# Optimization experiments

Hardware: AMD Instinct MI355X
Metric: run time of the kernel (lower is better)

Reference implementation:

```python
import jax, jax.numpy as jnp
import numpy as np

N_NODES = 50000
N_EDGES = 800000
HEADS = 2
HID = 64
NEG_SLOPE = 0.2


def setup_inputs() -> dict:
    key = jax.random.key(0)
    ks = jax.random.split(key, 8)
    x = jax.random.normal(ks[0], (N_NODES, 128), dtype=jnp.float32)
    W_src = jax.random.normal(ks[1], (128, HEADS * HID), dtype=jnp.float32) * (1.0 / np.sqrt(128))
    W_dst = jax.random.normal(ks[2], (128, HEADS * HID), dtype=jnp.float32) * (1.0 / np.sqrt(128))
    att_src = jax.random.normal(ks[3], (HEADS, HID), dtype=jnp.float32) * 0.1
    att_dst = jax.random.normal(ks[4], (HEADS, HID), dtype=jnp.float32) * 0.1
    bias = jax.random.normal(ks[5], (HEADS * HID,), dtype=jnp.float32) * 0.01
    prelu_w = jnp.full((HEADS * HID,), 0.25, dtype=jnp.float32)
    edge_index = jax.random.randint(ks[6], (2, N_EDGES), 0, N_NODES, dtype=jnp.int64)
    return {"x": x, "W_src": W_src, "W_dst": W_dst, "att_src": att_src,
            "att_dst": att_dst, "bias": bias, "prelu_w": prelu_w,
            "edge_index": edge_index}


def gat_prelu(x, W_src, W_dst, att_src, att_dst, bias, prelu_w, edge_index):
    N = x.shape[0]
    src, dst = edge_index[0], edge_index[1]
    xs = (x @ W_src).reshape(N, HEADS, HID)   # [N,H,C]
    xd = (x @ W_dst).reshape(N, HEADS, HID)
    a_src = jnp.einsum('nhc,hc->nh', xs, att_src)  # [N,H]
    a_dst = jnp.einsum('nhc,hc->nh', xd, att_dst)
    e = jax.nn.leaky_relu(a_src[src] + a_dst[dst], NEG_SLOPE)  # [E,H]
    # segment softmax over incoming edges of each dst node
    m = jax.ops.segment_max(e, dst, num_segments=N)            # [N,H]
    ee = jnp.exp(e - m[dst])
    denom = jax.ops.segment_sum(ee, dst, num_segments=N)
    alpha = ee / (denom[dst] + 1e-16)                          # [E,H]
    msg = xs[src] * alpha[:, :, None]                          # [E,H,C]
    out = jax.ops.segment_sum(msg, dst, num_segments=N)        # [N,H,C]
    out = out.reshape(N, HEADS * HID) + bias
    return jnp.where(out >= 0, out, prelu_w * out)


def reference(x, W_src, W_dst, att_src, att_dst, bias, prelu_w, edge_index):
    return gat_prelu(x, W_src, W_dst, att_src, att_dst, bias, prelu_w, edge_index)
```

## Files before the change

### kernel.cpp

```cpp
#include <hip/hip_runtime.h>
#include <hip/hip_fp16.h>


#define N_NODES 50000
#define N_EDGES 800000
#define CAP     56
#define BSH     8
#define NB      196
#define CHUNK   4096
#define NBLK    196
#define CCAP    64

#define OFF_A      0
#define OFF_CNT    800000
#define OFF_XS     1000256
#define OFF_BKT0   13800256
#define OFF_BKT1   25000256
#define OFF_SWZ    36200256
#define DOUT_COARSE 0
#define DOUT_CELL   19668992

typedef _Float16 f16x8 __attribute__((ext_vector_type(8)));
typedef _Float16 f16x4 __attribute__((ext_vector_type(4)));
typedef float    f32x4 __attribute__((ext_vector_type(4)));
typedef int      i32x4 __attribute__((ext_vector_type(4)));
typedef unsigned long long u64;

__global__ __launch_bounds__(256) void k0_prep(
    const float* __restrict__ Wsrc, const float* __restrict__ Wdst,
    const float* __restrict__ att_s, const float* __restrict__ att_d,
    __half* __restrict__ swz)
{
    __shared__ float vS[128 * 4];
    const int nt = blockIdx.x;
    const int t = threadIdx.x;
    if (nt == 8) {
        if (t < 128) {
            const float* wsp = Wsrc + t * 128;
            const float* wdp = Wdst + t * 128;
            float a0 = 0.f, a1 = 0.f, a2 = 0.f, a3 = 0.f;
#pragma unroll 8
            for (int c = 0; c < 64; ++c) {
                a0 += wsp[c]      * att_s[c];
                a1 += wsp[64 + c] * att_s[64 + c];
                a2 += wdp[c]      * att_d[c];
                a3 += wdp[64 + c] * att_d[64 + c];
            }
            *(float4*)(vS + t * 4) = make_float4(a0, a1, a2, a3);
        }
        __syncthreads();
    }
    const int kb = t >> 6, L = t & 63;
    const int col = L & 15;
    const int krow = kb * 32 + ((L >> 4) & 3) * 8;
    f16x8 v;
    if (nt < 8) {
#pragma unroll
        for (int j = 0; j < 8; ++j)
            v[j] = (_Float16)Wsrc[(size_t)(krow + j) * 128 + nt * 16 + col];
    } else {
#pragma unroll
        for (int j = 0; j < 8; ++j)
            v[j] = (col < 4) ? (_Float16)vS[(krow + j) * 4 + col] : (_Float16)0.f;
    }
    *(f16x8*)(swz + ((size_t)(kb * 9 + nt) * 64 + L) * 8) = v;
}

__global__ __launch_bounds__(256) void k1_gemm(
    const float* __restrict__ x, const __half* __restrict__ swz,
    __half* __restrict__ xs, float* __restrict__ a_all)
{
    __shared__ __half tile[64 * 136];
    const int t = threadIdx.x;
    const int w = t >> 6, L = t & 63;
    const int m = L & 15, q = L >> 4;
    const int n_a = blockIdx.x * 64 + w * 16 + m;
    const int rrow = (n_a < N_NODES) ? n_a : (N_NODES - 1);
    const float* xrow = x + (size_t)rrow * 128;

    f32x4 acc[9];
#pragma unroll
    for (int nt = 0; nt < 9; ++nt) acc[nt] = (f32x4){0.f, 0.f, 0.f, 0.f};

#pragma unroll
    for (int kb = 0; kb < 4; ++kb) {
        const int k0 = kb * 32 + q * 8;
        float4 xa = *(const float4*)(xrow + k0);
        float4 xb = *(const float4*)(xrow + k0 + 4);
        f16x8 a;
        a[0] = (_Float16)xa.x; a[1] = (_Float16)xa.y;
        a[2] = (_Float16)xa.z; a[3] = (_Float16)xa.w;
        a[4] = (_Float16)xb.x; a[5] = (_Float16)xb.y;
        a[6] = (_Float16)xb.z; a[7] = (_Float16)xb.w;
        const f16x8* bbase = (const f16x8*)swz + (size_t)(kb * 9) * 64 + L;
#pragma unroll
        for (int nt = 0; nt < 9; ++nt) {
            f16x8 b = bbase[(size_t)nt * 64];
            acc[nt] = __builtin_amdgcn_mfma_f32_16x16x32_f16(a, b, acc[nt], 0, 0, 0);
        }
    }

    const int rloc = w * 16 + q * 4;
#pragma unroll
    for (int nt = 0; nt < 8; ++nt) {
#pragma unroll
        for (int r = 0; r < 4; ++r)
            tile[(rloc + r) * 136 + nt * 16 + m] = (__half)acc[nt][r];
    }
    __syncthreads();
    const int n0 = blockIdx.x * 64;
#pragma unroll
    for (int cc = 0; cc < 4; ++cc) {
        int task = cc * 256 + t;
        int row = task >> 4, ch = task & 15;
        int n = n0 + row;
        if (n < N_NODES) {
            ulonglong2 v = *(const ulonglong2*)(tile + row * 136 + ch * 8);
            *(ulonglong2*)(xs + ((size_t)(ch >> 2) * N_NODES + n) * 32 + (ch & 3) * 8) = v;
        }
    }

    if (m < 4) {
#pragma unroll
        for (int r = 0; r < 4; ++r) {
            int n = n0 + rloc + r;
            if (n < N_NODES) a_all[(size_t)n * 4 + m] = acc[8][r];
        }
    }
}

__global__ __launch_bounds__(256) void kB_bin(
    const int* __restrict__ ei, const float* __restrict__ a_all,
    u64* __restrict__ coarse, int* __restrict__ cellcnt)
{
    __shared__ int lcnt[NB];
    const int t = threadIdx.x;
    if (t < NB) lcnt[t] = 0;
    __syncthreads();
    const int e0 = blockIdx.x * CHUNK;
#pragma unroll
    for (int u = 0; u < 8; ++u) {
        int e = e0 + u * 512 + t * 2;
        if (e < N_EDGES) {
            int2 ss = *(const int2*)(ei + e);
            int2 dd = *(const int2*)(ei + N_EDGES + e);
            float2 as0 = *(const float2*)(a_all + (size_t)ss.x * 4);
            float2 ad0 = *(const float2*)(a_all + (size_t)dd.x * 4 + 2);
            float2 as1 = *(const float2*)(a_all + (size_t)ss.y * 4);
            float2 ad1 = *(const float2*)(a_all + (size_t)dd.y * 4 + 2);
            float e00 = as0.x + ad0.x, e01 = as0.y + ad0.y;
            float e10 = as1.x + ad1.x, e11 = as1.y + ad1.y;
            e00 = (e00 >= 0.f) ? e00 : 0.2f * e00;
            e01 = (e01 >= 0.f) ? e01 : 0.2f * e01;
            e10 = (e10 >= 0.f) ? e10 : 0.2f * e10;
            e11 = (e11 >= 0.f) ? e11 : 0.2f * e11;
            __half2 hw0 = __floats2half2_rn(__expf(e00), __expf(e01));
            __half2 hw1 = __floats2half2_rn(__expf(e10), __expf(e11));
            unsigned lo0 = (unsigned)ss.x | ((unsigned)(dd.x & 255) << 16);
            unsigned lo1 = (unsigned)ss.y | ((unsigned)(dd.y & 255) << 16);
            u64 ent0 = (u64)lo0 | ((u64)*reinterpret_cast<unsigned*>(&hw0) << 32);
            u64 ent1 = (u64)lo1 | ((u64)*reinterpret_cast<unsigned*>(&hw1) << 32);
            int b0 = dd.x >> BSH, b1 = dd.y >> BSH;
            int p0 = atomicAdd(&lcnt[b0], 1);
            int p1 = atomicAdd(&lcnt[b1], 1);
            if (p0 < CCAP)
                coarse[((size_t)b0 * NBLK + blockIdx.x) * CCAP + p0] = ent0;
            if (p1 < CCAP)
                coarse[((size_t)b1 * NBLK + blockIdx.x) * CCAP + p1] = ent1;
        }
    }
    __syncthreads();
    if (t < NB) {
        int c = lcnt[t];
        cellcnt[t * NBLK + blockIdx.x] = (c < CCAP) ? c : CCAP;
    }
}

__global__ __launch_bounds__(512) void kD_fine(
    const u64* __restrict__ coarse, const int* __restrict__ cellcnt,
    int* __restrict__ cnt, int* __restrict__ bkt0, int* __restrict__ bkt1)
{
    __shared__ int cur[256];
    __shared__ int ccnt[NBLK];
    const int b = blockIdx.x, t = threadIdx.x;
    if (t < 256) cur[t] = 0;
    if (t < NBLK) ccnt[t] = cellcnt[b * NBLK + t];
    __syncthreads();
    const u64* src = coarse + (size_t)b * NBLK * CCAP;
    const int HALF = CCAP / 2;
    for (int g2 = t; g2 < NBLK * HALF; g2 += 512) {
        int c = g2 >> 5, sp = (g2 & 31) * 2;
        int cc = ccnt[c];
        if (sp < cc) {
            ulonglong2 pr = *(const ulonglong2*)(src + (size_t)c * CCAP + sp);
            {
                unsigned lo = (unsigned)pr.x;
                unsigned hw = (unsigned)(pr.x >> 32);
                int drel = (lo >> 16) & 255;
                int pos = atomicAdd(&cur[drel], 1);
                if (pos < CAP) {
                    int idx = ((b << BSH) + drel) * CAP + pos;
                    bkt0[idx] = (int)((lo & 0xFFFF) | (hw << 16));
                    bkt1[idx] = (int)((lo & 0xFFFF) | (hw & 0xFFFF0000u));
                }
            }
            if (sp + 1 < cc) {
                unsigned lo = (unsigned)pr.y;
                unsigned hw = (unsigned)(pr.y >> 32);
                int drel = (lo >> 16) & 255;
                int pos = atomicAdd(&cur[drel], 1);
                if (pos < CAP) {
                    int idx = ((b << BSH) + drel) * CAP + pos;
                    bkt0[idx] = (int)((lo & 0xFFFF) | (hw << 16));
                    bkt1[idx] = (int)((lo & 0xFFFF) | (hw & 0xFFFF0000u));
                }
            }
        }
    }
    __syncthreads();
    if (t < 256) {
        int d = (b << BSH) + t;
        if (d < N_NODES) {
            int c = cur[t];
            cnt[d] = c;
            int cc = (c < CAP) ? c : CAP;
            int ce = (cc + 7) & ~7;
            for (int p = cc; p < ce; ++p) {
                bkt0[d * CAP + p] = 0;
                bkt1[d * CAP + p] = 0;
            }
        }
    }
}

__global__ __launch_bounds__(256) void k6_pass(
    const int* __restrict__ bkt0, const int* __restrict__ bkt1,
    const int* __restrict__ cnt, const __half* __restrict__ xs,
    const float* __restrict__ bias, const float* __restrict__ prelu_w,
    float* __restrict__ out)
{
    const int pass = blockIdx.x & 3;
    const int grp  = blockIdx.x >> 2;
    const int t = threadIdx.x;
    const int w = t >> 6, lane = t & 63;
    const int l8 = lane & 7;
    const int node = grp * 32 + w * 8 + (lane >> 3);
    const int c4 = l8 * 4;
    const int j = pass * 32 + c4;
    const __half* xsp = xs + pass * (N_NODES * 32);
    const int* bk = (pass & 2) ? bkt1 : bkt0;

    const bool valid = (node < N_NODES);
    int m = 0;
    if (valid) { m = cnt[node]; if (m > CAP) m = CAP; }
    const int mr = (m + 7) & ~7;
    const i32x4* row = (const i32x4*)(bk + (valid ? node : 0) * CAP);

    float a0c = 0.f, a1c = 0.f, a2c = 0.f, a3c = 0.f, sw = 0.f;
    if (mr) {
        i32x4 e0 = row[0], e1 = row[1];
        int k = 0;
        for (;;) {
            const bool more = (k + 8 < mr);
            i32x4 f0, f1;
            if (more) {
                const i32x4* nr = row + ((k + 8) >> 2);
                f0 = nr[0]; f1 = nr[1];
            }
            f16x4 h0 = *(const f16x4*)(xsp + (e0[0] & 0xFFFF) * 32 + c4);
            f16x4 h1 = *(const f16x4*)(xsp + (e0[1] & 0xFFFF) * 32 + c4);
            f16x4 h2 = *(const f16x4*)(xsp + (e0[2] & 0xFFFF) * 32 + c4);
            f16x4 h3 = *(const f16x4*)(xsp + (e0[3] & 0xFFFF) * 32 + c4);
            f16x4 h4 = *(const f16x4*)(xsp + (e1[0] & 0xFFFF) * 32 + c4);
            f16x4 h5 = *(const f16x4*)(xsp + (e1[1] & 0xFFFF) * 32 + c4);
            f16x4 h6 = *(const f16x4*)(xsp + (e1[2] & 0xFFFF) * 32 + c4);
            f16x4 h7 = *(const f16x4*)(xsp + (e1[3] & 0xFFFF) * 32 + c4);
            float a0 = __half2float(__ushort_as_half((unsigned short)(((unsigned)e0[0]) >> 16)));
            float a1 = __half2float(__ushort_as_half((unsigned short)(((unsigned)e0[1]) >> 16)));
            float a2 = __half2float(__ushort_as_half((unsigned short)(((unsigned)e0[2]) >> 16)));
            float a3 = __half2float(__ushort_as_half((unsigned short)(((unsigned)e0[3]) >> 16)));
            float a4 = __half2float(__ushort_as_half((unsigned short)(((unsigned)e1[0]) >> 16)));
            float a5 = __half2float(__ushort_as_half((unsigned short)(((unsigned)e1[1]) >> 16)));
            float a6 = __half2float(__ushort_as_half((unsigned short)(((unsigned)e1[2]) >> 16)));
            float a7 = __half2float(__ushort_as_half((unsigned short)(((unsigned)e1[3]) >> 16)));
            a0c += (float)h0[0] * a0; a1c += (float)h0[1] * a0;
            a2c += (float)h0[2] * a0; a3c += (float)h0[3] * a0;
            a0c += (float)h1[0] * a1; a1c += (float)h1[1] * a1;
            a2c += (float)h1[2] * a1; a3c += (float)h1[3] * a1;
            a0c += (float)h2[0] * a2; a1c += (float)h2[1] * a2;
            a2c += (float)h2[2] * a2; a3c += (float)h2[3] * a2;
            a0c += (float)h3[0] * a3; a1c += (float)h3[1] * a3;
            a2c += (float)h3[2] * a3; a3c += (float)h3[3] * a3;
            a0c += (float)h4[0] * a4; a1c += (float)h4[1] * a4;
            a2c += (float)h4[2] * a4; a3c += (float)h4[3] * a4;
            a0c += (float)h5[0] * a5; a1c += (float)h5[1] * a5;
            a2c += (float)h5[2] * a5; a3c += (float)h5[3] * a5;
            a0c += (float)h6[0] * a6; a1c += (float)h6[1] * a6;
            a2c += (float)h6[2] * a6; a3c += (float)h6[3] * a6;
            a0c += (float)h7[0] * a7; a1c += (float)h7[1] * a7;
            a2c += (float)h7[2] * a7; a3c += (float)h7[3] * a7;
            sw += ((a0 + a1) + (a2 + a3)) + ((a4 + a5) + (a6 + a7));
            k += 8;
            if (k >= mr) break;
            e0 = f0; e1 = f1;
        }
    }

    if (valid) {
        const float4 bj = *(const float4*)(bias + j);
        const float4 pj = *(const float4*)(prelu_w + j);
        float inv = 1.f / (sw + 1e-16f);
        float o0 = a0c * inv + bj.x;
        float o1 = a1c * inv + bj.y;
        float o2 = a2c * inv + bj.z;
        float o3 = a3c * inv + bj.w;
        float4 r;
        r.x = (o0 >= 0.f) ? o0 : pj.x * o0;
        r.y = (o1 >= 0.f) ? o1 : pj.y * o1;
        r.z = (o2 >= 0.f) ? o2 : pj.z * o2;
        r.w = (o3 >= 0.f) ? o3 : pj.w * o3;
        *(float4*)(out + (size_t)node * 128 + j) = r;
    }
}

extern "C" void kernel_launch(void* const* d_in, const int* in_sizes, int n_in,
                              void* d_out, int out_size, void* d_ws, size_t ws_size,
                              hipStream_t stream) {
    const float* x      = (const float*)d_in[0];
    const float* Wsrc   = (const float*)d_in[1];
    const float* Wdst   = (const float*)d_in[2];
    const float* att_s  = (const float*)d_in[3];
    const float* att_d  = (const float*)d_in[4];
    const float* bias   = (const float*)d_in[5];
    const float* prelu  = (const float*)d_in[6];
    const int*   ei     = (const int*)d_in[7];
    float* out = (float*)d_out;

    char* ws = (char*)d_ws;
    float*  a_all  = (float*)(ws + OFF_A);
    int*    cnt    = (int*)(ws + OFF_CNT);
    __half* xs     = (__half*)(ws + OFF_XS);
    int*    bkt0   = (int*)(ws + OFF_BKT0);
    int*    bkt1   = (int*)(ws + OFF_BKT1);
    __half* swz    = (__half*)(ws + OFF_SWZ);

    char* outb = (char*)d_out;
    u64* coarse  = (u64*)(outb + DOUT_COARSE);
    int* cellcnt = (int*)(outb + DOUT_CELL);

    k0_prep<<<9, 256, 0, stream>>>(Wsrc, Wdst, att_s, att_d, swz);
    k1_gemm<<<(N_NODES + 63) / 64, 256, 0, stream>>>(x, swz, xs, a_all);
    kB_bin<<<NBLK, 256, 0, stream>>>(ei, a_all, coarse, cellcnt);
    kD_fine<<<NB, 512, 0, stream>>>(coarse, cellcnt, cnt, bkt0, bkt1);
    k6_pass<<<4 * ((N_NODES + 31) / 32), 256, 0, stream>>>(bkt0, bkt1, cnt, xs, bias, prelu, out);
}
```

Before: 166.2 us.

## Replace two-pass coarse/fine binning with direct global-atomic bucket scatter

Removes the coarse-bin kernel and the fine-bin kernel, and instead scatters each edge straight into its per-destination bucket using global atomicAdd on the count array. The count array is now zeroed inside the GEMM kernel. Because buckets are no longer zero-padded to a multiple of 8, the aggregation kernel gains a masked tail iteration for the leftover edges. This saves one kernel launch and the round trip through the intermediate coarse buffer. In exchange it pays for 800K contended global atomics and more scattered writes.

```diff
diff --git a/kernel.cpp b/kernel.cpp
--- a/kernel.cpp
+++ b/kernel.cpp
@@ -5,11 +5,6 @@
 #define N_NODES 50000
 #define N_EDGES 800000
 #define CAP     56
-#define BSH     8
-#define NB      196
-#define CHUNK   4096
-#define NBLK    196
-#define CCAP    64
 
 #define OFF_A      0
 #define OFF_CNT    800000
@@ -17,8 +12,6 @@
 #define OFF_BKT0   13800256
 #define OFF_BKT1   25000256
 #define OFF_SWZ    36200256
-#define DOUT_COARSE 0
-#define DOUT_CELL   19668992
 
 typedef _Float16 f16x8 __attribute__((ext_vector_type(8)));
 typedef _Float16 f16x4 __attribute__((ext_vector_type(4)));
@@ -68,7 +61,7 @@
 
 __global__ __launch_bounds__(256) void k1_gemm(
     const float* __restrict__ x, const __half* __restrict__ swz,
-    __half* __restrict__ xs, float* __restrict__ a_all)
+    __half* __restrict__ xs, float* __restrict__ a_all, int* __restrict__ cnt)
 {
     __shared__ __half tile[64 * 136];
     const int t = threadIdx.x;
@@ -77,6 +70,11 @@
     const int n_a = blockIdx.x * 64 + w * 16 + m;
     const int rrow = (n_a < N_NODES) ? n_a : (N_NODES - 1);
     const float* xrow = x + (size_t)rrow * 128;
+
+    if (t < 64) {
+        int n = blockIdx.x * 64 + t;
+        if (n < N_NODES) cnt[n] = 0;
+    }
 
     f32x4 acc[9];
 #pragma unroll
@@ -131,16 +129,12 @@
 
 __global__ __launch_bounds__(256) void kB_bin(
     const int* __restrict__ ei, const float* __restrict__ a_all,
-    u64* __restrict__ coarse, int* __restrict__ cellcnt)
+    int* __restrict__ cnt, int* __restrict__ bkt0, int* __restrict__ bkt1)
 {
-    __shared__ int lcnt[NB];
-    const int t = threadIdx.x;
-    if (t < NB) lcnt[t] = 0;
-    __syncthreads();
-    const int e0 = blockIdx.x * CHUNK;
-#pragma unroll
-    for (int u = 0; u < 8; ++u) {
-        int e = e0 + u * 512 + t * 2;
+    const int e0b = blockIdx.x * 2048;
+#pragma unroll
+    for (int u = 0; u < 4; ++u) {
+        int e = e0b + u * 512 + threadIdx.x * 2;
         if (e < N_EDGES) {
             int2 ss = *(const int2*)(ei + e);
             int2 dd = *(const int2*)(ei + N_EDGES + e);
@@ -156,78 +150,19 @@
             e11 = (e11 >= 0.f) ? e11 : 0.2f * e11;
             __half2 hw0 = __floats2half2_rn(__expf(e00), __expf(e01));
             __half2 hw1 = __floats2half2_rn(__expf(e10), __expf(e11));
-            unsigned lo0 = (unsigned)ss.x | ((unsigned)(dd.x & 255) << 16);
-            unsigned lo1 = (unsigned)ss.y | ((unsigned)(dd.y & 255) << 16);
-            u64 ent0 = (u64)lo0 | ((u64)*reinterpret_cast<unsigned*>(&hw0) << 32);
-            u64 ent1 = (u64)lo1 | ((u64)*reinterpret_cast<unsigned*>(&hw1) << 32);
-            int b0 = dd.x >> BSH, b1 = dd.y >> BSH;
-            int p0 = atomicAdd(&lcnt[b0], 1);
-            int p1 = atomicAdd(&lcnt[b1], 1);
-            if (p0 < CCAP)
-                coarse[((size_t)b0 * NBLK + blockIdx.x) * CCAP + p0] = ent0;
-            if (p1 < CCAP)
-                coarse[((size_t)b1 * NBLK + blockIdx.x) * CCAP + p1] = ent1;
-        }
-    }
-    __syncthreads();
-    if (t < NB) {
-        int c = lcnt[t];
-        cellcnt[t * NBLK + blockIdx.x] = (c < CCAP) ? c : CCAP;
-    }
-}
-
-__global__ __launch_bounds__(512) void kD_fine(
-    const u64* __restrict__ coarse, const int* __restrict__ cellcnt,
-    int* __restrict__ cnt, int* __restrict__ bkt0, int* __restrict__ bkt1)
-{
-    __shared__ int cur[256];
-    __shared__ int ccnt[NBLK];
-    const int b = blockIdx.x, t = threadIdx.x;
-    if (t < 256) cur[t] = 0;
-    if (t < NBLK) ccnt[t] = cellcnt[b * NBLK + t];
-    __syncthreads();
-    const u64* src = coarse + (size_t)b * NBLK * CCAP;
-    const int HALF = CCAP / 2;
-    for (int g2 = t; g2 < NBLK * HALF; g2 += 512) {
-        int c = g2 >> 5, sp = (g2 & 31) * 2;
-        int cc = ccnt[c];
-        if (sp < cc) {
-            ulonglong2 pr = *(const ulonglong2*)(src + (size_t)c * CCAP + sp);
-            {
-                unsigned lo = (unsigned)pr.x;
-                unsigned hw = (unsigned)(pr.x >> 32);
-                int drel = (lo >> 16) & 255;
-                int pos = atomicAdd(&cur[drel], 1);
-                if (pos < CAP) {
-                    int idx = ((b << BSH) + drel) * CAP + pos;
-                    bkt0[idx] = (int)((lo & 0xFFFF) | (hw << 16));
-                    bkt1[idx] = (int)((lo & 0xFFFF) | (hw & 0xFFFF0000u));
-                }
+            unsigned h0b = *reinterpret_cast<unsigned*>(&hw0);
+            unsigned h1b = *reinterpret_cast<unsigned*>(&hw1);
+            int p0 = atomicAdd(&cnt[dd.x], 1);
+            if (p0 < CAP) {
+                int idx = dd.x * CAP + p0;
+                bkt0[idx] = (int)((unsigned)ss.x | (h0b << 16));
+                bkt1[idx] = (int)((unsigned)ss.x | (h0b & 0xFFFF0000u));
             }
-            if (sp + 1 < cc) {
-                unsigned lo = (unsigned)pr.y;
-                unsigned hw = (unsigned)(pr.y >> 32);
-                int drel = (lo >> 16) & 255;
-                int pos = atomicAdd(&cur[drel], 1);
-                if (pos < CAP) {
-                    int idx = ((b << BSH) + drel) * CAP + pos;
-                    bkt0[idx] = (int)((lo & 0xFFFF) | (hw << 16));
-                    bkt1[idx] = (int)((lo & 0xFFFF) | (hw & 0xFFFF0000u));
-                }
-            }
-        }
-    }
-    __syncthreads();
-    if (t < 256) {
-        int d = (b << BSH) + t;
-        if (d < N_NODES) {
-            int c = cur[t];
-            cnt[d] = c;
-            int cc = (c < CAP) ? c : CAP;
-            int ce = (cc + 7) & ~7;
-            for (int p = cc; p < ce; ++p) {
-                bkt0[d * CAP + p] = 0;
-                bkt1[d * CAP + p] = 0;
+            int p1 = atomicAdd(&cnt[dd.y], 1);
+            if (p1 < CAP) {
+                int idx = dd.y * CAP + p1;
+                bkt0[idx] = (int)((unsigned)ss.y | (h1b << 16));
+                bkt1[idx] = (int)((unsigned)ss.y | (h1b & 0xFFFF0000u));
             }
         }
     }
@@ -253,15 +188,15 @@
     const bool valid = (node < N_NODES);
     int m = 0;
     if (valid) { m = cnt[node]; if (m > CAP) m = CAP; }
-    const int mr = (m + 7) & ~7;
     const i32x4* row = (const i32x4*)(bk + (valid ? node : 0) * CAP);
 
     float a0c = 0.f, a1c = 0.f, a2c = 0.f, a3c = 0.f, sw = 0.f;
-    if (mr) {
+    const int mf = m & ~7;
+    int k = 0;
+    if (mf) {
         i32x4 e0 = row[0], e1 = row[1];
-        int k = 0;
         for (;;) {
-            const bool more = (k + 8 < mr);
+            const bool more = (k + 8 < mf);
             i32x4 f0, f1;
             if (more) {
                 const i32x4* nr = row + ((k + 8) >> 2);
@@ -301,9 +236,53 @@
             a2c += (float)h7[2] * a7; a3c += (float)h7[3] * a7;
             sw += ((a0 + a1) + (a2 + a3)) + ((a4 + a5) + (a6 + a7));
             k += 8;
-            if (k >= mr) break;
+            if (k >= mf) break;
             e0 = f0; e1 = f1;
         }
+    }
+    if (k < m) {
+        i32x4 e0 = row[k >> 2], e1 = row[(k >> 2) + 1];
+        e0[0] = (k + 0 < m) ? e0[0] : 0;
+        e0[1] = (k + 1 < m) ? e0[1] : 0;
+        e0[2] = (k + 2 < m) ? e0[2] : 0;
+        e0[3] = (k + 3 < m) ? e0[3] : 0;
+        e1[0] = (k + 4 < m) ? e1[0] : 0;
+        e1[1] = (k + 5 < m) ? e1[1] : 0;
+        e1[2] = (k + 6 < m) ? e1[2] : 0;
+        e1[3] = (k + 7 < m) ? e1[3] : 0;
+        f16x4 h0 = *(const f16x4*)(xsp + (e0[0] & 0xFFFF) * 32 + c4);
+        f16x4 h1 = *(const f16x4*)(xsp + (e0[1] & 0xFFFF) * 32 + c4);
+        f16x4 h2 = *(const f16x4*)(xsp + (e0[2] & 0xFFFF) * 32 + c4);
+        f16x4 h3 = *(const f16x4*)(xsp + (e0[3] & 0xFFFF) * 32 + c4);
+        f16x4 h4 = *(const f16x4*)(xsp + (e1[0] & 0xFFFF) * 32 + c4);
+        f16x4 h5 = *(const f16x4*)(xsp + (e1[1] & 0xFFFF) * 32 + c4);
+        f16x4 h6 = *(const f16x4*)(xsp + (e1[2] & 0xFFFF) * 32 + c4);
+        f16x4 h7 = *(const f16x4*)(xsp + (e1[3] & 0xFFFF) * 32 + c4);
+        float a0 = __half2float(__ushort_as_half((unsigned short)(((unsigned)e0[0]) >> 16)));
+        float a1 = __half2float(__ushort_as_half((unsigned short)(((unsigned)e0[1]) >> 16)));
+        float a2 = __half2float(__ushort_as_half((unsigned short)(((unsigned)e0[2]) >> 16)));
+        float a3 = __half2float(__ushort_as_half((unsigned short)(((unsigned)e0[3]) >> 16)));
+        float a4 = __half2float(__ushort_as_half((unsigned short)(((unsigned)e1[0]) >> 16)));
+        float a5 = __half2float(__ushort_as_half((unsigned short)(((unsigned)e1[1]) >> 16)));
+        float a6 = __half2float(__ushort_as_half((unsigned short)(((unsigned)e1[2]) >> 16)));
+        float a7 = __half2float(__ushort_as_half((unsigned short)(((unsigned)e1[3]) >> 16)));
+        a0c += (float)h0[0] * a0; a1c += (float)h0[1] * a0;
+        a2c += (float)h0[2] * a0; a3c += (float)h0[3] * a0;
+        a0c += (float)h1[0] * a1; a1c += (float)h1[1] * a1;
+        a2c += (float)h1[2] * a1; a3c += (float)h1[3] * a1;
+        a0c += (float)h2[0] * a2; a1c += (float)h2[1] * a2;
+        a2c += (float)h2[2] * a2; a3c += (float)h2[3] * a2;
+        a0c += (float)h3[0] * a3; a1c += (float)h3[1] * a3;
+        a2c += (float)h3[2] * a3; a3c += (float)h3[3] * a3;
+        a0c += (float)h4[0] * a4; a1c += (float)h4[1] * a4;
+        a2c += (float)h4[2] * a4; a3c += (float)h4[3] * a4;
+        a0c += (float)h5[0] * a5; a1c += (float)h5[1] * a5;
+        a2c += (float)h5[2] * a5; a3c += (float)h5[3] * a5;
+        a0c += (float)h6[0] * a6; a1c += (float)h6[1] * a6;
+        a2c += (float)h6[2] * a6; a3c += (float)h6[3] * a6;
+        a0c += (float)h7[0] * a7; a1c += (float)h7[1] * a7;
+        a2c += (float)h7[2] * a7; a3c += (float)h7[3] * a7;
+        sw += ((a0 + a1) + (a2 + a3)) + ((a4 + a5) + (a6 + a7));
     }
 
     if (valid) {
@@ -344,13 +323,8 @@
     int*    bkt1   = (int*)(ws + OFF_BKT1);
     __half* swz    = (__half*)(ws + OFF_SWZ);
 
-    char* outb = (char*)d_out;
-    u64* coarse  = (u64*)(outb + DOUT_COARSE);
-    int* cellcnt = (int*)(outb + DOUT_CELL);
-
     k0_prep<<<9, 256, 0, stream>>>(Wsrc, Wdst, att_s, att_d, swz);
-    k1_gemm<<<(N_NODES + 63) / 64, 256, 0, stream>>>(x, swz, xs, a_all);
-    kB_bin<<<NBLK, 256, 0, stream>>>(ei, a_all, coarse, cellcnt);
-    kD_fine<<<NB, 512, 0, stream>>>(coarse, cellcnt, cnt, bkt0, bkt1);
+    k1_gemm<<<(N_NODES + 63) / 64, 256, 0, stream>>>(x, swz, xs, a_all, cnt);
+    kB_bin<<<392, 256, 0, stream>>>(ei, a_all, cnt, bkt0, bkt1);
     k6_pass<<<4 * ((N_NODES + 31) / 32), 256, 0, stream>>>(bkt0, bkt1, cnt, xs, bias, prelu, out);
 }
```

After: 181.8 us. +9.4%, slower.
